# Kernel tuning notes

Measured on AMD Instinct MI355X. Metric: run time of the kernel, lower is better.

## Reference

```python
import jax, jax.numpy as jnp
import numpy as np

LOG_2PI = np.float32(np.log(2.0 * np.pi))


def setup_inputs() -> dict:
    key = jax.random.key(0)
    k1, k2, k3 = jax.random.split(key, 3)
    shape = (16, 1024, 10, 2, 50)  # (bs, seq_len, N_art, 2, N_samples)
    mean_ = jax.random.normal(k1, shape, dtype=jnp.float32)
    # variances must be strictly positive
    var_ = jax.random.uniform(k2, shape, dtype=jnp.float32) + jnp.float32(0.1)
    targets_ = jax.random.normal(k3, shape, dtype=jnp.float32)
    return {"mean_": mean_, "var_": var_, "targets_": targets_}


def reference(mean_, var_, targets_):
    # Diagonal 2x2 Gaussian NLL, closed form (equivalent to the
    # MultivariateNormal cholesky path with a diagonal covariance):
    #   -log p(x) = 0.5 * sum_d [ (x_d - mu_d)^2 / var_d + log var_d ] + log(2*pi)
    # Axis 3 (size 2) is the coordinate dimension d.
    diff = targets_ - mean_
    nll = 0.5 * jnp.sum(diff * diff / var_ + jnp.log(var_), axis=3) + LOG_2PI
    return jnp.mean(nll)  # reduction='mean'
```

## Files before the change

### kernel.cpp

```cpp
#include <hip/hip_runtime.h>
#include <hip/hip_bf16.h>

#define LOG_2PI 1.8378770664093453f

#define NBLOCKS 2048
#define NTHREADS 256

__global__ void __launch_bounds__(NTHREADS)
nll_partial_kernel(const float* __restrict__ mean_,
                   const float* __restrict__ var_,
                   const float* __restrict__ tgt_,
                   float* __restrict__ partial,
                   int n) {
    const int nvec = n >> 2;
    const int tid = blockIdx.x * blockDim.x + threadIdx.x;
    const int stride = gridDim.x * blockDim.x;

    const float4* m4 = reinterpret_cast<const float4*>(mean_);
    const float4* v4 = reinterpret_cast<const float4*>(var_);
    const float4* t4 = reinterpret_cast<const float4*>(tgt_);

    float s = 0.0f;
    for (int i = tid; i < nvec; i += stride) {
        float4 m = m4[i];
        float4 v = v4[i];
        float4 t = t4[i];
        float d0 = t.x - m.x;
        float d1 = t.y - m.y;
        float d2 = t.z - m.z;
        float d3 = t.w - m.w;
        s += d0 * d0 * __frcp_rn(v.x) + __logf(v.x);
        s += d1 * d1 * __frcp_rn(v.y) + __logf(v.y);
        s += d2 * d2 * __frcp_rn(v.z) + __logf(v.z);
        s += d3 * d3 * __frcp_rn(v.w) + __logf(v.w);
    }

    if (tid == 0) {
        for (int i = nvec << 2; i < n; ++i) {
            float d = tgt_[i] - mean_[i];
            s += d * d * __frcp_rn(var_[i]) + __logf(var_[i]);
        }
    }

    #pragma unroll
    for (int off = 32; off > 0; off >>= 1)
        s += __shfl_down(s, off, 64);

    __shared__ float smem[NTHREADS / 64];
    const int wave = threadIdx.x >> 6;
    if ((threadIdx.x & 63) == 0) smem[wave] = s;
    __syncthreads();
    if (threadIdx.x == 0) {
        float b = 0.0f;
        #pragma unroll
        for (int w = 0; w < NTHREADS / 64; ++w) b += smem[w];
        partial[blockIdx.x] = b;
    }
}

__global__ void __launch_bounds__(NTHREADS)
nll_final_kernel(const float* __restrict__ partial,
                 float* __restrict__ out,
                 int nb, float inv_n) {
    float s = 0.0f;
    for (int i = threadIdx.x; i < nb; i += blockDim.x)
        s += partial[i];

    #pragma unroll
    for (int off = 32; off > 0; off >>= 1)
        s += __shfl_down(s, off, 64);

    __shared__ float smem[NTHREADS / 64];
    const int wave = threadIdx.x >> 6;
    if ((threadIdx.x & 63) == 0) smem[wave] = s;
    __syncthreads();
    if (threadIdx.x == 0) {
        float b = 0.0f;
        #pragma unroll
        for (int w = 0; w < NTHREADS / 64; ++w) b += smem[w];
        out[0] = b * inv_n + LOG_2PI;
    }
}

extern "C" void kernel_launch(void* const* d_in, const int* in_sizes, int n_in,
                              void* d_out, int out_size, void* d_ws, size_t ws_size,
                              hipStream_t stream) {
    const float* mean_ = (const float*)d_in[0];
    const float* var_  = (const float*)d_in[1];
    const float* tgt_  = (const float*)d_in[2];
    float* out = (float*)d_out;
    float* partial = (float*)d_ws;

    const int n = in_sizes[0];

    nll_partial_kernel<<<NBLOCKS, NTHREADS, 0, stream>>>(mean_, var_, tgt_, partial, n);
    nll_final_kernel<<<1, NTHREADS, 0, stream>>>(partial, out, NBLOCKS, 1.0f / (float)n);
}
```

Baseline: 38.58 us.

## Fuse final reduction via last-block atomic counter and fully unroll exact-fit loop

Merges the two-kernel reduction into one kernel: each block publishes its partial sum with a release store, bumps an atomic counter, and the last block to arrive sums all partials and writes the result. The grid is resized to 2000 blocks so the 4M float4 elements split into exactly eight per thread, which enables a fully unrolled path using two accumulators. The correctly rounded reciprocal is replaced with the hardware approximate rcp. In exchange the kernel needs a memset of the counter before each launch and an atomic handshake per block.

New measurement: 153.6 us. +298.1%, slower.

```diff
diff --git a/kernel.cpp b/kernel.cpp
--- a/kernel.cpp
+++ b/kernel.cpp
@@ -3,82 +3,107 @@
 
 #define LOG_2PI 1.8378770664093453f
 
-#define NBLOCKS 2048
+#define NBLOCKS 2000
 #define NTHREADS 256
 
+__device__ __forceinline__ float nll_elem4(const float4 m, const float4 v, const float4 t) {
+    float d0 = t.x - m.x;
+    float d1 = t.y - m.y;
+    float d2 = t.z - m.z;
+    float d3 = t.w - m.w;
+    float s;
+    s  = d0 * d0 * __builtin_amdgcn_rcpf(v.x) + __logf(v.x);
+    s += d1 * d1 * __builtin_amdgcn_rcpf(v.y) + __logf(v.y);
+    s += d2 * d2 * __builtin_amdgcn_rcpf(v.z) + __logf(v.z);
+    s += d3 * d3 * __builtin_amdgcn_rcpf(v.w) + __logf(v.w);
+    return s;
+}
+
 __global__ void __launch_bounds__(NTHREADS)
-nll_partial_kernel(const float* __restrict__ mean_,
-                   const float* __restrict__ var_,
-                   const float* __restrict__ tgt_,
-                   float* __restrict__ partial,
-                   int n) {
+nll_fused_kernel(const float* __restrict__ mean_,
+                 const float* __restrict__ var_,
+                 const float* __restrict__ tgt_,
+                 float* __restrict__ partial,
+                 unsigned int* __restrict__ counter,
+                 float* __restrict__ out,
+                 int n, float inv_n) {
     const int nvec = n >> 2;
     const int tid = blockIdx.x * blockDim.x + threadIdx.x;
     const int stride = gridDim.x * blockDim.x;
 
-    const float4* m4 = reinterpret_cast<const float4*>(mean_);
-    const float4* v4 = reinterpret_cast<const float4*>(var_);
-    const float4* t4 = reinterpret_cast<const float4*>(tgt_);
+    const float4* __restrict__ m4 = reinterpret_cast<const float4*>(mean_);
+    const float4* __restrict__ v4 = reinterpret_cast<const float4*>(var_);
+    const float4* __restrict__ t4 = reinterpret_cast<const float4*>(tgt_);
 
-    float s = 0.0f;
-    for (int i = tid; i < nvec; i += stride) {
-        float4 m = m4[i];
-        float4 v = v4[i];
-        float4 t = t4[i];
-        float d0 = t.x - m.x;
-        float d1 = t.y - m.y;
-        float d2 = t.z - m.z;
-        float d3 = t.w - m.w;
-        s += d0 * d0 * __frcp_rn(v.x) + __logf(v.x);
-        s += d1 * d1 * __frcp_rn(v.y) + __logf(v.y);
-        s += d2 * d2 * __frcp_rn(v.z) + __logf(v.z);
-        s += d3 * d3 * __frcp_rn(v.w) + __logf(v.w);
-    }
+    float s0 = 0.0f, s1 = 0.0f;
 
-    if (tid == 0) {
-        for (int i = nvec << 2; i < n; ++i) {
-            float d = tgt_[i] - mean_[i];
-            s += d * d * __frcp_rn(var_[i]) + __logf(var_[i]);
+    if (nvec == stride * 8 && (n & 3) == 0) {
+        #pragma unroll
+        for (int k = 0; k < 8; k += 2) {
+            const int i = tid + k * stride;
+            const int j = i + stride;
+            float4 ma = m4[i], va = v4[i], ta = t4[i];
+            float4 mb = m4[j], vb = v4[j], tb = t4[j];
+            s0 += nll_elem4(ma, va, ta);
+            s1 += nll_elem4(mb, vb, tb);
+        }
+    } else {
+        int i = tid;
+        for (; i + stride < nvec; i += 2 * stride) {
+            const int j = i + stride;
+            float4 ma = m4[i], va = v4[i], ta = t4[i];
+            float4 mb = m4[j], vb = v4[j], tb = t4[j];
+            s0 += nll_elem4(ma, va, ta);
+            s1 += nll_elem4(mb, vb, tb);
+        }
+        if (i < nvec) s0 += nll_elem4(m4[i], v4[i], t4[i]);
+        if (tid == 0) {
+            for (int k = nvec << 2; k < n; ++k) {
+                float d = tgt_[k] - mean_[k];
+                s0 += d * d * __builtin_amdgcn_rcpf(var_[k]) + __logf(var_[k]);
+            }
         }
     }
 
+    float s = s0 + s1;
     #pragma unroll
     for (int off = 32; off > 0; off >>= 1)
         s += __shfl_down(s, off, 64);
 
     __shared__ float smem[NTHREADS / 64];
-    const int wave = threadIdx.x >> 6;
-    if ((threadIdx.x & 63) == 0) smem[wave] = s;
+    __shared__ bool amLast;
+    if ((threadIdx.x & 63) == 0) smem[threadIdx.x >> 6] = s;
     __syncthreads();
+
     if (threadIdx.x == 0) {
         float b = 0.0f;
         #pragma unroll
         for (int w = 0; w < NTHREADS / 64; ++w) b += smem[w];
-        partial[blockIdx.x] = b;
+        __hip_atomic_store(&partial[blockIdx.x], b, __ATOMIC_RELEASE,
+                           __HIP_MEMORY_SCOPE_AGENT);
+        unsigned int prev = __hip_atomic_fetch_add(counter, 1u, __ATOMIC_ACQ_REL,
+                                                   __HIP_MEMORY_SCOPE_AGENT);
+        amLast = (prev == (unsigned int)(gridDim.x - 1));
     }
-}
+    __syncthreads();
 
-__global__ void __launch_bounds__(NTHREADS)
-nll_final_kernel(const float* __restrict__ partial,
-                 float* __restrict__ out,
-                 int nb, float inv_n) {
-    float s = 0.0f;
-    for (int i = threadIdx.x; i < nb; i += blockDim.x)
-        s += partial[i];
-
-    #pragma unroll
-    for (int off = 32; off > 0; off >>= 1)
-        s += __shfl_down(s, off, 64);
-
-    __shared__ float smem[NTHREADS / 64];
-    const int wave = threadIdx.x >> 6;
-    if ((threadIdx.x & 63) == 0) smem[wave] = s;
-    __syncthreads();
-    if (threadIdx.x == 0) {
-        float b = 0.0f;
+    if (amLast) {
+        float t = 0.0f;
+        for (int j = threadIdx.x; j < (int)gridDim.x; j += (int)blockDim.x)
+            t += __hip_atomic_load(&partial[j], __ATOMIC_RELAXED,
+                                   __HIP_MEMORY_SCOPE_AGENT);
         #pragma unroll
-        for (int w = 0; w < NTHREADS / 64; ++w) b += smem[w];
-        out[0] = b * inv_n + LOG_2PI;
+        for (int off = 32; off > 0; off >>= 1)
+            t += __shfl_down(t, off, 64);
+        __shared__ float smem2[NTHREADS / 64];
+        if ((threadIdx.x & 63) == 0) smem2[threadIdx.x >> 6] = t;
+        __syncthreads();
+        if (threadIdx.x == 0) {
+            float b = 0.0f;
+            #pragma unroll
+            for (int w = 0; w < NTHREADS / 64; ++w) b += smem2[w];
+            out[0] = b * inv_n + LOG_2PI;
+        }
     }
 }
 
@@ -89,10 +114,14 @@
     const float* var_  = (const float*)d_in[1];
     const float* tgt_  = (const float*)d_in[2];
     float* out = (float*)d_out;
+
     float* partial = (float*)d_ws;
+    unsigned int* counter =
+        (unsigned int*)((char*)d_ws + NBLOCKS * sizeof(float));
 
     const int n = in_sizes[0];
 
-    nll_partial_kernel<<<NBLOCKS, NTHREADS, 0, stream>>>(mean_, var_, tgt_, partial, n);
-    nll_final_kernel<<<1, NTHREADS, 0, stream>>>(partial, out, NBLOCKS, 1.0f / (float)n);
+    hipMemsetAsync(counter, 0, sizeof(unsigned int), stream);
+    nll_fused_kernel<<<NBLOCKS, NTHREADS, 0, stream>>>(
+        mean_, var_, tgt_, partial, counter, out, n, 1.0f / (float)n);
 }
```
